# Optimization experiments

Measured on AMD Instinct MI355X. Metric: run time of the kernel, lower is better.

Reference implementation:

```python
import jax, jax.numpy as jnp
import numpy as np

CHUNK = 64  # chunk_size
EPS = 1e-6


def setup_inputs() -> dict:
    key = jax.random.key(0)
    ks = jax.random.split(key, 7)
    b, L, H, dh, ds = 2, 4096, 16, 64, 64
    X = jax.random.normal(ks[0], (b, L, H, dh), dtype=jnp.float32)
    # negative log-decay in (-1, 0) for numerical stability (Mamba2 convention)
    A = -jax.random.uniform(ks[1], (b, L, H), dtype=jnp.float32)
    B = jax.random.normal(ks[2], (b, L, H, ds), dtype=jnp.float32)
    C = jax.random.normal(ks[3], (b, L, H, ds), dtype=jnp.float32)
    log2_alpha_base = jnp.full((H,), -0.15, dtype=jnp.float32) + 0.02 * jax.random.normal(ks[4], (H,), dtype=jnp.float32)
    log2_beta = 0.02 * jax.random.normal(ks[5], (H,), dtype=jnp.float32)
    surprise_ema = jnp.ones((H,), dtype=jnp.float32)
    return {"X": X, "A": A, "B": B, "C": C,
            "log2_alpha_base": log2_alpha_base, "log2_beta": log2_beta,
            "surprise_ema": surprise_ema}


def reference(X, A, B, C, log2_alpha_base, log2_beta, surprise_ema):
    b, L, H, dh = X.shape
    ds = B.shape[-1]
    n = L // CHUNK  # L is a multiple of CHUNK (no padding needed)

    # [b, h, n, c, ...] layout
    Xt = X.reshape(b, n, CHUNK, H, dh).transpose(0, 3, 1, 2, 4)   # b h n c dh
    At = A.reshape(b, n, CHUNK, H).transpose(0, 3, 1, 2)          # b h n c
    Bt = B.reshape(b, n, CHUNK, H, ds).transpose(0, 3, 1, 2, 4)   # b h n c ds
    Ct = C.reshape(b, n, CHUNK, H, ds).transpose(0, 3, 1, 2, 4)   # b h n c ds

    # per-chunk surprise from outer-product state delta
    BX = jnp.einsum('bhncs,bhncd->bhnsd', Bt, Xt)                 # b h n ds dh
    chunk_surprise = (BX ** 2).mean(axis=(-1, -2))                # b h n

    # surprise gate (eval mode: EMA buffer not updated)
    normalized = chunk_surprise / (surprise_ema[None, :, None] + EPS)
    log2c = jnp.clip(log2_alpha_base, -3.32, -0.015)
    alpha_base = 1.0 - jnp.exp2(log2c)                            # [H]
    beta = jnp.exp2(jnp.clip(log2_beta, -2.0, 2.0))               # [H]
    boost = jax.nn.relu(jnp.tanh(beta[None, :, None] * normalized))
    alpha = jnp.clip(alpha_base[None, :, None]
                     + (1.0 - alpha_base[None, :, None]) * boost, 0.01, 0.999)

    # surprise-modulated decay
    A_mod = At * (1.0 - alpha)[..., None]                         # b h n c
    A_cs = jnp.cumsum(A_mod, axis=-1)                             # b h n c

    # intra-chunk attention-like term with causal decay matrix
    diff = A_cs[..., :, None] - A_cs[..., None, :]                # b h n c c
    causal = jnp.tril(jnp.ones((CHUNK, CHUNK), dtype=bool))
    Lmat = jnp.where(causal, jnp.exp(diff), 0.0)
    CB = jnp.einsum('bhnid,bhnjd->bhnij', Ct, Bt)
    Y_intra = jnp.einsum('bhnij,bhnjd->bhnid', Lmat * CB, Xt)

    # inter-chunk state carry (sequential over chunks)
    decay_chunk = jnp.exp(A_mod.sum(axis=-1))                     # b h n
    decay_to_end = jnp.exp(A_cs[..., -1:] - A_cs)                 # b h n c
    h_final = jnp.einsum('bhnc,bhncs,bhncd->bhnsd', decay_to_end, Bt, Xt)

    def step(carry, inp):
        dc, hf = inp                                              # dc: b h ; hf: b h ds dh
        return dc[..., None, None] * carry + hf, carry

    dc_n = jnp.moveaxis(decay_chunk, 2, 0)                        # n b h
    hf_n = jnp.moveaxis(h_final, 2, 0)                            # n b h ds dh
    init = jnp.zeros((b, H, ds, dh), X.dtype)
    _, h_inter_n = jax.lax.scan(step, init, (dc_n, hf_n))
    h_inter = jnp.moveaxis(h_inter_n, 0, 2)                       # b h n ds dh

    decay_from_start = jnp.exp(A_cs)
    Y_inter = jnp.einsum('bhnis,bhnsp,bhni->bhnip', Ct, h_inter, decay_from_start)

    Y = (Y_intra + Y_inter).transpose(0, 2, 3, 1, 4).reshape(b, L, H, dh)
    return Y
```

## Files before the change

kernel.cpp:

```cpp
#include <hip/hip_runtime.h>
#include <hip/hip_bf16.h>
#include <math.h>

#define LSEQ 4096
#define NH   16
#define DH   64
#define CH   64
#define NCH  64
#define LDT  72

typedef __attribute__((ext_vector_type(8))) short bf16x8;
typedef __attribute__((ext_vector_type(4))) short s16x4;
typedef __attribute__((ext_vector_type(4))) float f32x4;

#define MFMA16(a, b, c) __builtin_amdgcn_mfma_f32_16x16x32_bf16((a), (b), (c), 0, 0, 0)

__device__ __forceinline__ float4 ld4(const float* p) {
    return *reinterpret_cast<const float4*>(p);
}
__device__ __forceinline__ short f2b(float x) {
    __hip_bfloat16 h = __float2bfloat16(x);
    return *reinterpret_cast<short*>(&h);
}
__device__ __forceinline__ float b2f(short s) {
    union { unsigned u; float f; } v;
    v.u = ((unsigned)(unsigned short)s) << 16;
    return v.f;
}
__device__ __forceinline__ s16x4 pack4(float a, float b, float c, float d) {
    s16x4 r; r.x = f2b(a); r.y = f2b(b); r.z = f2b(c); r.w = f2b(d); return r;
}
__device__ __forceinline__ uint2 sx2(uint2 v, int m) {
    uint2 r;
    r.x = (unsigned)__shfl_xor((int)v.x, m, 64);
    r.y = (unsigned)__shfl_xor((int)v.y, m, 64);
    return r;
}
__device__ __forceinline__ short ext4(uint2 u, int g) {
    unsigned word = (g & 2) ? u.y : u.x;
    return (short)((g & 1) ? (word >> 16) : (word & 0xffffu));
}

__global__ __launch_bounds__(256) void ssd_k1(
    const float* __restrict__ X, const float* __restrict__ A,
    const float* __restrict__ B, const float* __restrict__ C,
    const float* __restrict__ l2ab, const float* __restrict__ l2b,
    const float* __restrict__ ema,
    unsigned short* __restrict__ yw, unsigned short* __restrict__ hf,
    float* __restrict__ dcb, float* __restrict__ dfs)
{
    __shared__ __align__(16) short R1[CH * LDT];
    __shared__ __align__(16) short R2[CH * LDT];
    __shared__ __align__(16) short R3[CH * LDT];
    __shared__ __align__(16) float red[4];

    const int tid  = threadIdx.x;
    const int blk  = blockIdx.x;
    const int nidx = blk & (NCH - 1);
    const int h    = (blk >> 6) & (NH - 1);
    const int bb   = blk >> 10;
    const size_t base = ((size_t)(bb * LSEQ + nidx * CH) * NH + h) * DH;

    const int lane = tid & 63;
    const int w    = tid >> 6;
    const int rb   = 16 * w;
    const int fr   = lane & 15;
    const int gq   = lane >> 4;
    const int g4   = 4 * gq;
    const int ko   = 8 * gq;

    #pragma unroll
    for (int m = 0; m < 4; ++m) {
        int p = tid + 256 * m;
        int c = p >> 4, d0 = (p & 15) * 4;
        size_t g = base + (size_t)c * 1024 + d0;
        float4 xv = ld4(&X[g]);
        float4 bv = ld4(&B[g]);
        float4 cv = ld4(&C[g]);
        *reinterpret_cast<s16x4*>(&R1[c * LDT + d0]) = pack4(xv.x, xv.y, xv.z, xv.w);
        *reinterpret_cast<s16x4*>(&R2[c * LDT + d0]) = pack4(bv.x, bv.y, bv.z, bv.w);
        *reinterpret_cast<s16x4*>(&R3[c * LDT + d0]) = pack4(cv.x, cv.y, cv.z, cv.w);
    }
    float aval = A[(size_t)(bb * LSEQ + nidx * CH + lane) * NH + h];
    __syncthreads();

    const f32x4 zf = {0.f, 0.f, 0.f, 0.f};

    f32x4 aGX[4] = {zf, zf, zf, zf};
    f32x4 aGB[4] = {zf, zf, zf, zf};
    f32x4 aCB[4] = {zf, zf, zf, zf};
    #pragma unroll
    for (int k0 = 0; k0 < 64; k0 += 32) {
        bf16x8 aX = *reinterpret_cast<const bf16x8*>(&R1[(rb + fr) * LDT + k0 + ko]);
        bf16x8 aB = *reinterpret_cast<const bf16x8*>(&R2[(rb + fr) * LDT + k0 + ko]);
        bf16x8 aC = *reinterpret_cast<const bf16x8*>(&R3[(rb + fr) * LDT + k0 + ko]);
        #pragma unroll
        for (int n = 0; n < 4; ++n) {
            bf16x8 bX = *reinterpret_cast<const bf16x8*>(&R1[(16 * n + fr) * LDT + k0 + ko]);
            bf16x8 bB = *reinterpret_cast<const bf16x8*>(&R2[(16 * n + fr) * LDT + k0 + ko]);
            aGX[n] = MFMA16(aX, bX, aGX[n]);
            aGB[n] = MFMA16(aB, bB, aGB[n]);
            aCB[n] = MFMA16(aC, bB, aCB[n]);
        }
    }
    float ss = 0.f;
    #pragma unroll
    for (int n = 0; n < 4; ++n)
        #pragma unroll
        for (int r = 0; r < 4; ++r) ss += aGX[n][r] * aGB[n][r];
    #pragma unroll
    for (int off = 32; off > 0; off >>= 1) ss += __shfl_down(ss, off, 64);
    if (lane == 0) red[w] = ss;
    __syncthreads();

    float4 rv = *reinterpret_cast<const float4*>(red);
    float surprise = (rv.x + rv.y + rv.z + rv.w) * (1.f / 4096.f);
    float l2c   = fminf(fmaxf(l2ab[h], -3.32f), -0.015f);
    float ab_   = 1.f - exp2f(l2c);
    float bt    = exp2f(fminf(fmaxf(l2b[h], -2.f), 2.f));
    float nrm   = surprise / (ema[h] + 1e-6f);
    float boost = fmaxf(tanhf(bt * nrm), 0.f);
    float alpha = fminf(fmaxf(ab_ + (1.f - ab_) * boost, 0.01f), 0.999f);
    float scale = 1.f - alpha;
    float v = aval * scale;
    #pragma unroll
    for (int off = 1; off < 64; off <<= 1) {
        float t = __shfl_up(v, off, 64);
        if (lane >= off) v += t;
    }
    float tot  = __shfl(v, 63, 64);
    float epv  = __expf(v);
    float env  = __expf(-v);
    float dtev = __expf(tot - v);
    if (w == 0) {
        dfs[(size_t)blk * CH + lane] = epv;
        if (lane == 63) dcb[blk] = __expf(tot);
    }

    {
        float epi[4], enj[4];
        #pragma unroll
        for (int r = 0; r < 4; ++r) epi[r] = __shfl(epv, rb + g4 + r, 64);
        #pragma unroll
        for (int n = 0; n < 4; ++n) enj[n] = __shfl(env, 16 * n + fr, 64);
        #pragma unroll
        for (int n = 0; n < 4; ++n)
            #pragma unroll
            for (int r = 0; r < 4; ++r) {
                int i = rb + g4 + r, j = 16 * n + fr;
                float val = (j <= i) ? epi[r] * enj[n] * aCB[n][r] : 0.f;
                R3[i * LDT + j] = f2b(val);
            }
    }

    s16x4 outX[4], outB[4];
    const int d0 = 4 * fr;
    #pragma unroll
    for (int m = 0; m < 4; ++m) {
        int c0 = 16 * w + 4 * m;
        uint2 mx = *reinterpret_cast<const uint2*>(&R1[(c0 + gq) * LDT + d0]);
        uint2 mb = *reinterpret_cast<const uint2*>(&R2[(c0 + gq) * LDT + d0]);
        uint2 px = sx2(mx, 16), pb = sx2(mb, 16);
        uint2 xe = (gq & 1) ? px : mx, xo = (gq & 1) ? mx : px;
        uint2 be = (gq & 1) ? pb : mb, bo = (gq & 1) ? mb : pb;
        uint2 xpe = sx2(xe, 32), xpo = sx2(xo, 32);
        uint2 bpe = sx2(be, 32), bpo = sx2(bo, 32);
        uint2 xr0 = (gq & 2) ? xpe : xe, xr1 = (gq & 2) ? xpo : xo;
        uint2 xr2 = (gq & 2) ? xe : xpe, xr3 = (gq & 2) ? xo : xpo;
        uint2 br0 = (gq & 2) ? bpe : be, br1 = (gq & 2) ? bpo : bo;
        uint2 br2 = (gq & 2) ? be : bpe, br3 = (gq & 2) ? bo : bpo;
        s16x4 ox; ox.x = ext4(xr0, gq); ox.y = ext4(xr1, gq);
                  ox.z = ext4(xr2, gq); ox.w = ext4(xr3, gq);
        outX[m] = ox;
        float dt0 = __shfl(dtev, c0 + 0, 64), dt1 = __shfl(dtev, c0 + 1, 64);
        float dt2 = __shfl(dtev, c0 + 2, 64), dt3 = __shfl(dtev, c0 + 3, 64);
        s16x4 ob;
        ob.x = f2b(b2f(ext4(br0, gq)) * dt0);
        ob.y = f2b(b2f(ext4(br1, gq)) * dt1);
        ob.z = f2b(b2f(ext4(br2, gq)) * dt2);
        ob.w = f2b(b2f(ext4(br3, gq)) * dt3);
        outB[m] = ob;
    }
    __syncthreads();

    #pragma unroll
    for (int m = 0; m < 4; ++m) {
        int c0 = 16 * w + 4 * m;
        *reinterpret_cast<s16x4*>(&R1[(d0 + gq) * LDT + c0]) = outX[m];
        *reinterpret_cast<s16x4*>(&R2[(d0 + gq) * LDT + c0]) = outB[m];
    }
    __syncthreads();

    f32x4 acc2[4] = {zf, zf, zf, zf};
    f32x4 acc3[4] = {zf, zf, zf, zf};
    #pragma unroll
    for (int k0 = 0; k0 < 64; k0 += 32) {
        bf16x8 aX = *reinterpret_cast<const bf16x8*>(&R1[(rb + fr) * LDT + k0 + ko]);
        bf16x8 aB = *reinterpret_cast<const bf16x8*>(&R2[(rb + fr) * LDT + k0 + ko]);
        #pragma unroll
        for (int n = 0; n < 4; ++n) {
            bf16x8 bT = *reinterpret_cast<const bf16x8*>(&R3[(16 * n + fr) * LDT + k0 + ko]);
            bf16x8 bX = *reinterpret_cast<const bf16x8*>(&R1[(16 * n + fr) * LDT + k0 + ko]);
            acc2[n] = MFMA16(aX, bT, acc2[n]);
            acc3[n] = MFMA16(aB, bX, acc3[n]);
        }
    }
    #pragma unroll
    for (int n = 0; n < 4; ++n) {
        int colI = 16 * n + fr;
        s16x4 y4 = pack4(acc2[n][0], acc2[n][1], acc2[n][2], acc2[n][3]);
        s16x4 h4 = pack4(acc3[n][0], acc3[n][1], acc3[n][2], acc3[n][3]);
        *reinterpret_cast<s16x4*>(&yw[(size_t)blk * 4096 + colI * 64 + rb + g4]) = y4;
        *reinterpret_cast<s16x4*>(&hf[(size_t)blk * 4096 + colI * 64 + rb + g4]) = h4;
    }
}

__global__ __launch_bounds__(256) void ssd_k2(
    unsigned int* __restrict__ hfU, const float* __restrict__ dcb)
{
    __shared__ float sdc[NCH];
    const int tid = threadIdx.x;
    const int bh  = blockIdx.x >> 3;
    const int sub = blockIdx.x & 7;
    if (tid < NCH) sdc[tid] = dcb[bh * NCH + tid];
    __syncthreads();
    const size_t base = (size_t)bh * NCH * 2048 + sub * 256 + tid;

    float c0 = 0.f, c1 = 0.f;
    unsigned int cur[8];
    #pragma unroll
    for (int kk = 0; kk < 8; ++kk) cur[kk] = hfU[base + (size_t)kk * 2048];
    #pragma unroll
    for (int kb = 0; kb < 8; ++kb) {
        unsigned int nxt[8];
        if (kb < 7) {
            #pragma unroll
            for (int kk = 0; kk < 8; ++kk)
                nxt[kk] = hfU[base + (size_t)(8 * kb + 8 + kk) * 2048];
        }
        #pragma unroll
        for (int kk = 0; kk < 8; ++kk) {
            int k = 8 * kb + kk;
            unsigned int u = cur[kk];
            union { unsigned int q; float f; } lo, hi;
            lo.q = u << 16;
            hi.q = u & 0xffff0000u;
            unsigned int packed = (unsigned int)(unsigned short)f2b(c0)
                                | ((unsigned int)(unsigned short)f2b(c1) << 16);
            hfU[base + (size_t)k * 2048] = packed;
            float d = sdc[k];
            c0 = fmaf(d, c0, lo.f);
            c1 = fmaf(d, c1, hi.f);
        }
        if (kb < 7) {
            #pragma unroll
            for (int kk = 0; kk < 8; ++kk) cur[kk] = nxt[kk];
        }
    }
}

__global__ __launch_bounds__(256) void ssd_k3(
    const float* __restrict__ C, const unsigned short* __restrict__ hI,
    const unsigned short* __restrict__ yw, const float* __restrict__ dfs,
    float* __restrict__ Y)
{
    __shared__ __align__(16) short sHt[CH * LDT];
    __shared__ __align__(16) short sC2[CH * LDT];
    __shared__ float sF[CH];

    const int tid  = threadIdx.x;
    const int blk  = blockIdx.x;
    const int nidx = blk & (NCH - 1);
    const int h    = (blk >> 6) & (NH - 1);
    const int bb   = blk >> 10;
    const size_t base = ((size_t)(bb * LSEQ + nidx * CH) * NH + h) * DH;

    #pragma unroll
    for (int m = 0; m < 2; ++m) {
        int idx = tid + 256 * m;
        int row = idx >> 3, c8 = (idx & 7) * 8;
        bf16x8 v = *reinterpret_cast<const bf16x8*>(&hI[(size_t)blk * 4096 + row * 64 + c8]);
        *reinterpret_cast<bf16x8*>(&sHt[row * LDT + c8]) = v;
    }
    #pragma unroll
    for (int m = 0; m < 4; ++m) {
        int p = tid + 256 * m;
        int row = p >> 4, d0 = (p & 15) * 4;
        float4 cv = ld4(&C[base + (size_t)row * 1024 + d0]);
        *reinterpret_cast<s16x4*>(&sC2[row * LDT + d0]) = pack4(cv.x, cv.y, cv.z, cv.w);
    }
    if (tid < CH) sF[tid] = dfs[(size_t)blk * CH + tid];
    __syncthreads();

    const int lane = tid & 63;
    const int w    = tid >> 6;
    const int rb   = 16 * w;
    const int fr   = lane & 15;
    const int g4   = 4 * (lane >> 4);
    const int ko   = 8 * (lane >> 4);
    const f32x4 zf = {0.f, 0.f, 0.f, 0.f};

    f32x4 acc[4] = {zf, zf, zf, zf};
    #pragma unroll
    for (int k0 = 0; k0 < 64; k0 += 32) {
        bf16x8 a = *reinterpret_cast<const bf16x8*>(&sHt[(rb + fr) * LDT + k0 + ko]);
        #pragma unroll
        for (int n = 0; n < 4; ++n) {
            bf16x8 b = *reinterpret_cast<const bf16x8*>(&sC2[(16 * n + fr) * LDT + k0 + ko]);
            acc[n] = MFMA16(a, b, acc[n]);
        }
    }
    #pragma unroll
    for (int n = 0; n < 4; ++n) {
        int i  = 16 * n + fr;
        int p0 = rb + g4;
        float f = sF[i];
        const unsigned short* ywp = &yw[(size_t)blk * 4096 + i * 64 + p0];
        float4 o;
        o.x = fmaf(f, acc[n][0], b2f((short)ywp[0]));
        o.y = fmaf(f, acc[n][1], b2f((short)ywp[1]));
        o.z = fmaf(f, acc[n][2], b2f((short)ywp[2]));
        o.w = fmaf(f, acc[n][3], b2f((short)ywp[3]));
        *reinterpret_cast<float4*>(&Y[base + (size_t)i * 1024 + p0]) = o;
    }
}

extern "C" void kernel_launch(void* const* d_in, const int* in_sizes, int n_in,
                              void* d_out, int out_size, void* d_ws, size_t ws_size,
                              hipStream_t stream)
{
    const float* X    = (const float*)d_in[0];
    const float* A    = (const float*)d_in[1];
    const float* B    = (const float*)d_in[2];
    const float* C    = (const float*)d_in[3];
    const float* l2ab = (const float*)d_in[4];
    const float* l2b  = (const float*)d_in[5];
    const float* ema  = (const float*)d_in[6];
    float* Y = (float*)d_out;

    unsigned short* hf = (unsigned short*)d_ws;
    unsigned short* yw = hf + (size_t)8388608;
    float* dcb = (float*)(yw + (size_t)8388608);
    float* dfs = dcb + 2048;

    const int nblk = 2 * NH * NCH;
    ssd_k1<<<nblk, 256, 0, stream>>>(X, A, B, C, l2ab, l2b, ema, yw, hf, dcb, dfs);
    ssd_k2<<<256, 256, 0, stream>>>((unsigned int*)hf, dcb);
    ssd_k3<<<nblk, 256, 0, stream>>>(C, hf, yw, dfs, Y);
}
```

Measured before the change: 57.97 us.

## Process two chunks per block in k1 with register prefetch of next chunk

Each k1 block now handles two consecutive chunks, prefetching the second chunk's X/B/C/A into registers while the first chunk is being computed, which hides global load latency. Barriers become explicit lgkmcnt waits plus s_barrier, the Gram MFMAs are restructured so per-n accumulators are reduced immediately to cut register pressure, and launch bounds request 4 blocks per CU. The transpose-write loop order is rotated per lane group to spread LDS bank access. The cost is half as many blocks, which lowers parallelism, plus extra live registers for the prefetch.

```diff
diff --git a/kernel.cpp b/kernel.cpp
--- a/kernel.cpp
+++ b/kernel.cpp
@@ -40,8 +40,14 @@
     unsigned word = (g & 2) ? u.y : u.x;
     return (short)((g & 1) ? (word >> 16) : (word & 0xffffu));
 }
-
-__global__ __launch_bounds__(256) void ssd_k1(
+__device__ __forceinline__ void barrier_lds() {
+    __builtin_amdgcn_sched_barrier(0);
+    asm volatile("s_waitcnt lgkmcnt(0)" ::: "memory");
+    __builtin_amdgcn_s_barrier();
+    __builtin_amdgcn_sched_barrier(0);
+}
+
+__global__ __launch_bounds__(256, 4) void ssd_k1(
     const float* __restrict__ X, const float* __restrict__ A,
     const float* __restrict__ B, const float* __restrict__ C,
     const float* __restrict__ l2ab, const float* __restrict__ l2b,
@@ -54,12 +60,11 @@
     __shared__ __align__(16) short R3[CH * LDT];
     __shared__ __align__(16) float red[4];
 
-    const int tid  = threadIdx.x;
-    const int blk  = blockIdx.x;
-    const int nidx = blk & (NCH - 1);
-    const int h    = (blk >> 6) & (NH - 1);
-    const int bb   = blk >> 10;
-    const size_t base = ((size_t)(bb * LSEQ + nidx * CH) * NH + h) * DH;
+    const int tid   = threadIdx.x;
+    const int blk   = blockIdx.x;
+    const int npair = blk & 31;
+    const int h     = (blk >> 5) & (NH - 1);
+    const int bb    = blk >> 9;
 
     const int lane = tid & 63;
     const int w    = tid >> 6;
@@ -68,150 +73,179 @@
     const int gq   = lane >> 4;
     const int g4   = 4 * gq;
     const int ko   = 8 * gq;
-
-    #pragma unroll
-    for (int m = 0; m < 4; ++m) {
-        int p = tid + 256 * m;
-        int c = p >> 4, d0 = (p & 15) * 4;
-        size_t g = base + (size_t)c * 1024 + d0;
-        float4 xv = ld4(&X[g]);
-        float4 bv = ld4(&B[g]);
-        float4 cv = ld4(&C[g]);
-        *reinterpret_cast<s16x4*>(&R1[c * LDT + d0]) = pack4(xv.x, xv.y, xv.z, xv.w);
-        *reinterpret_cast<s16x4*>(&R2[c * LDT + d0]) = pack4(bv.x, bv.y, bv.z, bv.w);
-        *reinterpret_cast<s16x4*>(&R3[c * LDT + d0]) = pack4(cv.x, cv.y, cv.z, cv.w);
-    }
-    float aval = A[(size_t)(bb * LSEQ + nidx * CH + lane) * NH + h];
-    __syncthreads();
+    const int rot  = (fr >> 1) & 3;
+
+    const int sc = tid >> 4, sd0 = (tid & 15) * 4;
+
+    float4 px[4], pb[4], pc[4];
+    float  pa;
+
+    {
+        const int gc = 2 * npair;
+        const size_t bg = ((size_t)(bb * LSEQ + gc * CH) * NH + h) * DH;
+        #pragma unroll
+        for (int m = 0; m < 4; ++m) {
+            size_t g = bg + (size_t)(sc + 16 * m) * 1024 + sd0;
+            px[m] = ld4(&X[g]); pb[m] = ld4(&B[g]); pc[m] = ld4(&C[g]);
+        }
+        pa = A[(size_t)(bb * LSEQ + gc * CH + lane) * NH + h];
+    }
 
     const f32x4 zf = {0.f, 0.f, 0.f, 0.f};
 
-    f32x4 aGX[4] = {zf, zf, zf, zf};
-    f32x4 aGB[4] = {zf, zf, zf, zf};
-    f32x4 aCB[4] = {zf, zf, zf, zf};
-    #pragma unroll
-    for (int k0 = 0; k0 < 64; k0 += 32) {
-        bf16x8 aX = *reinterpret_cast<const bf16x8*>(&R1[(rb + fr) * LDT + k0 + ko]);
-        bf16x8 aB = *reinterpret_cast<const bf16x8*>(&R2[(rb + fr) * LDT + k0 + ko]);
-        bf16x8 aC = *reinterpret_cast<const bf16x8*>(&R3[(rb + fr) * LDT + k0 + ko]);
+    #pragma unroll
+    for (int it = 0; it < 2; ++it) {
+        const int gc   = 2 * npair + it;
+        const int gblk = ((bb * NH + h) << 6) | gc;
+        const size_t bg = ((size_t)(bb * LSEQ + gc * CH) * NH + h) * DH;
+
+        if (it) barrier_lds();
+
+        float aval = pa;
+        #pragma unroll
+        for (int m = 0; m < 4; ++m) {
+            int c = sc + 16 * m;
+            *reinterpret_cast<s16x4*>(&R1[c * LDT + sd0]) = pack4(px[m].x, px[m].y, px[m].z, px[m].w);
+            *reinterpret_cast<s16x4*>(&R2[c * LDT + sd0]) = pack4(pb[m].x, pb[m].y, pb[m].z, pb[m].w);
+            *reinterpret_cast<s16x4*>(&R3[c * LDT + sd0]) = pack4(pc[m].x, pc[m].y, pc[m].z, pc[m].w);
+        }
+        if (it == 0) {
+            const int gn = 2 * npair + 1;
+            const size_t bn = ((size_t)(bb * LSEQ + gn * CH) * NH + h) * DH;
+            #pragma unroll
+            for (int m = 0; m < 4; ++m) {
+                size_t g = bn + (size_t)(sc + 16 * m) * 1024 + sd0;
+                px[m] = ld4(&X[g]); pb[m] = ld4(&B[g]); pc[m] = ld4(&C[g]);
+            }
+            pa = A[(size_t)(bb * LSEQ + gn * CH + lane) * NH + h];
+        }
+        barrier_lds();
+
+        bf16x8 aX0 = *reinterpret_cast<const bf16x8*>(&R1[(rb + fr) * LDT + 0  + ko]);
+        bf16x8 aX1 = *reinterpret_cast<const bf16x8*>(&R1[(rb + fr) * LDT + 32 + ko]);
+        bf16x8 aB0 = *reinterpret_cast<const bf16x8*>(&R2[(rb + fr) * LDT + 0  + ko]);
+        bf16x8 aB1 = *reinterpret_cast<const bf16x8*>(&R2[(rb + fr) * LDT + 32 + ko]);
+        bf16x8 aC0 = *reinterpret_cast<const bf16x8*>(&R3[(rb + fr) * LDT + 0  + ko]);
+        bf16x8 aC1 = *reinterpret_cast<const bf16x8*>(&R3[(rb + fr) * LDT + 32 + ko]);
+        f32x4 aCB[4];
+        float ss = 0.f;
         #pragma unroll
         for (int n = 0; n < 4; ++n) {
-            bf16x8 bX = *reinterpret_cast<const bf16x8*>(&R1[(16 * n + fr) * LDT + k0 + ko]);
-            bf16x8 bB = *reinterpret_cast<const bf16x8*>(&R2[(16 * n + fr) * LDT + k0 + ko]);
-            aGX[n] = MFMA16(aX, bX, aGX[n]);
-            aGB[n] = MFMA16(aB, bB, aGB[n]);
-            aCB[n] = MFMA16(aC, bB, aCB[n]);
-        }
-    }
-    float ss = 0.f;
-    #pragma unroll
-    for (int n = 0; n < 4; ++n)
-        #pragma unroll
-        for (int r = 0; r < 4; ++r) ss += aGX[n][r] * aGB[n][r];
-    #pragma unroll
-    for (int off = 32; off > 0; off >>= 1) ss += __shfl_down(ss, off, 64);
-    if (lane == 0) red[w] = ss;
-    __syncthreads();
-
-    float4 rv = *reinterpret_cast<const float4*>(red);
-    float surprise = (rv.x + rv.y + rv.z + rv.w) * (1.f / 4096.f);
-    float l2c   = fminf(fmaxf(l2ab[h], -3.32f), -0.015f);
-    float ab_   = 1.f - exp2f(l2c);
-    float bt    = exp2f(fminf(fmaxf(l2b[h], -2.f), 2.f));
-    float nrm   = surprise / (ema[h] + 1e-6f);
-    float boost = fmaxf(tanhf(bt * nrm), 0.f);
-    float alpha = fminf(fmaxf(ab_ + (1.f - ab_) * boost, 0.01f), 0.999f);
-    float scale = 1.f - alpha;
-    float v = aval * scale;
-    #pragma unroll
-    for (int off = 1; off < 64; off <<= 1) {
-        float t = __shfl_up(v, off, 64);
-        if (lane >= off) v += t;
-    }
-    float tot  = __shfl(v, 63, 64);
-    float epv  = __expf(v);
-    float env  = __expf(-v);
-    float dtev = __expf(tot - v);
-    if (w == 0) {
-        dfs[(size_t)blk * CH + lane] = epv;
-        if (lane == 63) dcb[blk] = __expf(tot);
-    }
-
-    {
-        float epi[4], enj[4];
-        #pragma unroll
-        for (int r = 0; r < 4; ++r) epi[r] = __shfl(epv, rb + g4 + r, 64);
-        #pragma unroll
-        for (int n = 0; n < 4; ++n) enj[n] = __shfl(env, 16 * n + fr, 64);
-        #pragma unroll
-        for (int n = 0; n < 4; ++n)
-            #pragma unroll
-            for (int r = 0; r < 4; ++r) {
-                int i = rb + g4 + r, j = 16 * n + fr;
-                float val = (j <= i) ? epi[r] * enj[n] * aCB[n][r] : 0.f;
-                R3[i * LDT + j] = f2b(val);
+            bf16x8 bX0 = *reinterpret_cast<const bf16x8*>(&R1[(16 * n + fr) * LDT + 0  + ko]);
+            bf16x8 bX1 = *reinterpret_cast<const bf16x8*>(&R1[(16 * n + fr) * LDT + 32 + ko]);
+            bf16x8 bB0 = *reinterpret_cast<const bf16x8*>(&R2[(16 * n + fr) * LDT + 0  + ko]);
+            bf16x8 bB1 = *reinterpret_cast<const bf16x8*>(&R2[(16 * n + fr) * LDT + 32 + ko]);
+            f32x4 gx = MFMA16(aX1, bX1, MFMA16(aX0, bX0, zf));
+            f32x4 gb = MFMA16(aB1, bB1, MFMA16(aB0, bB0, zf));
+            aCB[n]   = MFMA16(aC1, bB1, MFMA16(aC0, bB0, zf));
+            #pragma unroll
+            for (int r = 0; r < 4; ++r) ss = fmaf(gx[r], gb[r], ss);
+        }
+        #pragma unroll
+        for (int off = 32; off > 0; off >>= 1) ss += __shfl_down(ss, off, 64);
+        if (lane == 0) red[w] = ss;
+        barrier_lds();
+
+        float4 rv = *reinterpret_cast<const float4*>(red);
+        float surprise = (rv.x + rv.y + rv.z + rv.w) * (1.f / 4096.f);
+        float l2c   = fminf(fmaxf(l2ab[h], -3.32f), -0.015f);
+        float ab_   = 1.f - exp2f(l2c);
+        float bt    = exp2f(fminf(fmaxf(l2b[h], -2.f), 2.f));
+        float nrm   = surprise / (ema[h] + 1e-6f);
+        float boost = fmaxf(tanhf(bt * nrm), 0.f);
+        float alpha = fminf(fmaxf(ab_ + (1.f - ab_) * boost, 0.01f), 0.999f);
+        float scale = 1.f - alpha;
+        float v = aval * scale;
+        #pragma unroll
+        for (int off = 1; off < 64; off <<= 1) {
+            float t = __shfl_up(v, off, 64);
+            if (lane >= off) v += t;
+        }
+        float tot  = __shfl(v, 63, 64);
+        float epv  = __expf(v);
+        float env  = __expf(-v);
+        float dtev = __expf(tot - v);
+        if (w == 0) {
+            dfs[(size_t)gblk * CH + lane] = epv;
+            if (lane == 63) dcb[gblk] = __expf(tot);
+        }
+
+        {
+            float epi[4], enj[4];
+            #pragma unroll
+            for (int r = 0; r < 4; ++r) epi[r] = __shfl(epv, rb + g4 + r, 64);
+            #pragma unroll
+            for (int n = 0; n < 4; ++n) enj[n] = __shfl(env, 16 * n + fr, 64);
+            #pragma unroll
+            for (int n = 0; n < 4; ++n)
+                #pragma unroll
+                for (int r = 0; r < 4; ++r) {
+                    int i = rb + g4 + r, j = 16 * n + fr;
+                    float val = (j <= i) ? epi[r] * enj[n] * aCB[n][r] : 0.f;
+                    R3[i * LDT + j] = f2b(val);
+                }
+        }
+
+        s16x4 outX[4], outB[4];
+        const int d0 = 4 * fr;
+        #pragma unroll
+        for (int m = 0; m < 4; ++m) {
+            int c0 = 16 * w + 4 * ((m + rot) & 3);
+            uint2 mx = *reinterpret_cast<const uint2*>(&R1[(c0 + gq) * LDT + d0]);
+            uint2 mb = *reinterpret_cast<const uint2*>(&R2[(c0 + gq) * LDT + d0]);
+            uint2 px_ = sx2(mx, 16), pb_ = sx2(mb, 16);
+            uint2 xe = (gq & 1) ? px_ : mx, xo = (gq & 1) ? mx : px_;
+            uint2 be = (gq & 1) ? pb_ : mb, bo = (gq & 1) ? mb : pb_;
+            uint2 xpe = sx2(xe, 32), xpo = sx2(xo, 32);
+            uint2 bpe = sx2(be, 32), bpo = sx2(bo, 32);
+            uint2 xr0 = (gq & 2) ? xpe : xe, xr1 = (gq & 2) ? xpo : xo;
+            uint2 xr2 = (gq & 2) ? xe : xpe, xr3 = (gq & 2) ? xo : xpo;
+            uint2 br0 = (gq & 2) ? bpe : be, br1 = (gq & 2) ? bpo : bo;
+            uint2 br2 = (gq & 2) ? be : bpe, br3 = (gq & 2) ? bo : bpo;
+            s16x4 ox; ox.x = ext4(xr0, gq); ox.y = ext4(xr1, gq);
+                      ox.z = ext4(xr2, gq); ox.w = ext4(xr3, gq);
+            outX[m] = ox;
+            float dt0 = __shfl(dtev, c0 + 0, 64), dt1 = __shfl(dtev, c0 + 1, 64);
+            float dt2 = __shfl(dtev, c0 + 2, 64), dt3 = __shfl(dtev, c0 + 3, 64);
+            s16x4 ob;
+            ob.x = f2b(b2f(ext4(br0, gq)) * dt0);
+            ob.y = f2b(b2f(ext4(br1, gq)) * dt1);
+            ob.z = f2b(b2f(ext4(br2, gq)) * dt2);
+            ob.w = f2b(b2f(ext4(br3, gq)) * dt3);
+            outB[m] = ob;
+        }
+        barrier_lds();
+
+        #pragma unroll
+        for (int m = 0; m < 4; ++m) {
+            int c0 = 16 * w + 4 * ((m + rot) & 3);
+            *reinterpret_cast<s16x4*>(&R1[(d0 + gq) * LDT + c0]) = outX[m];
+            *reinterpret_cast<s16x4*>(&R2[(d0 + gq) * LDT + c0]) = outB[m];
+        }
+        barrier_lds();
+
+        f32x4 acc2[4] = {zf, zf, zf, zf};
+        f32x4 acc3[4] = {zf, zf, zf, zf};
+        #pragma unroll
+        for (int k0 = 0; k0 < 64; k0 += 32) {
+            bf16x8 aX = *reinterpret_cast<const bf16x8*>(&R1[(rb + fr) * LDT + k0 + ko]);
+            bf16x8 aB = *reinterpret_cast<const bf16x8*>(&R2[(rb + fr) * LDT + k0 + ko]);
+            #pragma unroll
+            for (int n = 0; n < 4; ++n) {
+                bf16x8 bT = *reinterpret_cast<const bf16x8*>(&R3[(16 * n + fr) * LDT + k0 + ko]);
+                bf16x8 bX = *reinterpret_cast<const bf16x8*>(&R1[(16 * n + fr) * LDT + k0 + ko]);
+                acc2[n] = MFMA16(aX, bT, acc2[n]);
+                acc3[n] = MFMA16(aB, bX, acc3[n]);
             }
-    }
-
-    s16x4 outX[4], outB[4];
-    const int d0 = 4 * fr;
-    #pragma unroll
-    for (int m = 0; m < 4; ++m) {
-        int c0 = 16 * w + 4 * m;
-        uint2 mx = *reinterpret_cast<const uint2*>(&R1[(c0 + gq) * LDT + d0]);
-        uint2 mb = *reinterpret_cast<const uint2*>(&R2[(c0 + gq) * LDT + d0]);
-        uint2 px = sx2(mx, 16), pb = sx2(mb, 16);
-        uint2 xe = (gq & 1) ? px : mx, xo = (gq & 1) ? mx : px;
-        uint2 be = (gq & 1) ? pb : mb, bo = (gq & 1) ? mb : pb;
-        uint2 xpe = sx2(xe, 32), xpo = sx2(xo, 32);
-        uint2 bpe = sx2(be, 32), bpo = sx2(bo, 32);
-        uint2 xr0 = (gq & 2) ? xpe : xe, xr1 = (gq & 2) ? xpo : xo;
-        uint2 xr2 = (gq & 2) ? xe : xpe, xr3 = (gq & 2) ? xo : xpo;
-        uint2 br0 = (gq & 2) ? bpe : be, br1 = (gq & 2) ? bpo : bo;
-        uint2 br2 = (gq & 2) ? be : bpe, br3 = (gq & 2) ? bo : bpo;
-        s16x4 ox; ox.x = ext4(xr0, gq); ox.y = ext4(xr1, gq);
-                  ox.z = ext4(xr2, gq); ox.w = ext4(xr3, gq);
-        outX[m] = ox;
-        float dt0 = __shfl(dtev, c0 + 0, 64), dt1 = __shfl(dtev, c0 + 1, 64);
-        float dt2 = __shfl(dtev, c0 + 2, 64), dt3 = __shfl(dtev, c0 + 3, 64);
-        s16x4 ob;
-        ob.x = f2b(b2f(ext4(br0, gq)) * dt0);
-        ob.y = f2b(b2f(ext4(br1, gq)) * dt1);
-        ob.z = f2b(b2f(ext4(br2, gq)) * dt2);
-        ob.w = f2b(b2f(ext4(br3, gq)) * dt3);
-        outB[m] = ob;
-    }
-    __syncthreads();
-
-    #pragma unroll
-    for (int m = 0; m < 4; ++m) {
-        int c0 = 16 * w + 4 * m;
-        *reinterpret_cast<s16x4*>(&R1[(d0 + gq) * LDT + c0]) = outX[m];
-        *reinterpret_cast<s16x4*>(&R2[(d0 + gq) * LDT + c0]) = outB[m];
-    }
-    __syncthreads();
-
-    f32x4 acc2[4] = {zf, zf, zf, zf};
-    f32x4 acc3[4] = {zf, zf, zf, zf};
-    #pragma unroll
-    for (int k0 = 0; k0 < 64; k0 += 32) {
-        bf16x8 aX = *reinterpret_cast<const bf16x8*>(&R1[(rb + fr) * LDT + k0 + ko]);
-        bf16x8 aB = *reinterpret_cast<const bf16x8*>(&R2[(rb + fr) * LDT + k0 + ko]);
+        }
         #pragma unroll
         for (int n = 0; n < 4; ++n) {
-            bf16x8 bT = *reinterpret_cast<const bf16x8*>(&R3[(16 * n + fr) * LDT + k0 + ko]);
-            bf16x8 bX = *reinterpret_cast<const bf16x8*>(&R1[(16 * n + fr) * LDT + k0 + ko]);
-            acc2[n] = MFMA16(aX, bT, acc2[n]);
-            acc3[n] = MFMA16(aB, bX, acc3[n]);
-        }
-    }
-    #pragma unroll
-    for (int n = 0; n < 4; ++n) {
-        int colI = 16 * n + fr;
-        s16x4 y4 = pack4(acc2[n][0], acc2[n][1], acc2[n][2], acc2[n][3]);
-        s16x4 h4 = pack4(acc3[n][0], acc3[n][1], acc3[n][2], acc3[n][3]);
-        *reinterpret_cast<s16x4*>(&yw[(size_t)blk * 4096 + colI * 64 + rb + g4]) = y4;
-        *reinterpret_cast<s16x4*>(&hf[(size_t)blk * 4096 + colI * 64 + rb + g4]) = h4;
+            int colI = 16 * n + fr;
+            s16x4 y4 = pack4(acc2[n][0], acc2[n][1], acc2[n][2], acc2[n][3]);
+            s16x4 h4 = pack4(acc3[n][0], acc3[n][1], acc3[n][2], acc3[n][3]);
+            *reinterpret_cast<s16x4*>(&yw[(size_t)gblk * 4096 + colI * 64 + rb + g4]) = y4;
+            *reinterpret_cast<s16x4*>(&hf[(size_t)gblk * 4096 + colI * 64 + rb + g4]) = h4;
+        }
     }
 }
 
@@ -343,8 +377,7 @@
     float* dcb = (float*)(yw + (size_t)8388608);
     float* dfs = dcb + 2048;
 
-    const int nblk = 2 * NH * NCH;
-    ssd_k1<<<nblk, 256, 0, stream>>>(X, A, B, C, l2ab, l2b, ema, yw, hf, dcb, dfs);
+    ssd_k1<<<1024, 256, 0, stream>>>(X, A, B, C, l2ab, l2b, ema, yw, hf, dcb, dfs);
     ssd_k2<<<256, 256, 0, stream>>>((unsigned int*)hf, dcb);
-    ssd_k3<<<nblk, 256, 0, stream>>>(C, hf, yw, dfs, Y);
-}
+    ssd_k3<<<2048, 256, 0, stream>>>(C, hf, yw, dfs, Y);
+}
```

Result: slower. 67.45 us (+16.4%).
